# Kernel tuning notes

Measured on AMD Instinct MI355X. Metric: run time of the kernel, lower is better.

## Reference

```python
import jax, jax.numpy as jnp
import numpy as np

HID, FFN, NE, TOPK = 1024, 4096, 8, 2


def setup_inputs() -> dict:
    key = jax.random.key(0)
    ks = jax.random.split(key, 4)
    x = jax.random.normal(ks[0], (2, 2048, HID), dtype=jnp.float32)
    # router: nn.Linear(hidden, num_experts, bias=False), init std=0.02; stored as [H, E]
    Wr = jax.random.normal(ks[1], (HID, NE), dtype=jnp.float32) * 0.02
    # per-expert FFN weights stacked on leading expert axis
    W1 = jax.random.normal(ks[2], (NE, HID, FFN), dtype=jnp.float32) * (1.0 / np.sqrt(HID))
    b1 = jnp.zeros((NE, FFN), dtype=jnp.float32)
    W2 = jax.random.normal(ks[3], (NE, FFN, HID), dtype=jnp.float32) * (1.0 / np.sqrt(FFN))
    b2 = jnp.zeros((NE, HID), dtype=jnp.float32)
    return {"x": x, "Wr": Wr, "W1": W1, "b1": b1, "W2": W2, "b2": b2}


def reference(x, Wr, W1, b1, W2, b2):
    B, S, H = x.shape
    E = Wr.shape[1]
    T = B * S
    xf = x.reshape(T, H)                                  # [T, H]
    logits = xf @ Wr                                      # [T, E]
    probs = jax.nn.softmax(logits, axis=-1)
    topk_p, topk_i = jax.lax.top_k(probs, TOPK)           # [T, K]
    topk_p = topk_p / jnp.sum(topk_p, axis=-1, keepdims=True)
    # dense combine weights: c[t, e] = normalized prob if expert e selected for token t else 0
    c = jnp.zeros((T, E), dtype=xf.dtype).at[jnp.arange(T)[:, None], topk_i].add(topk_p)

    def expert_step(acc, ew):
        w1, bb1, w2, bb2, ce = ew                         # ce: [T]
        h = jax.nn.gelu(xf @ w1 + bb1, approximate=False)  # exact GELU like nn.GELU()
        y = h @ w2 + bb2                                  # [T, H]
        return acc + ce[:, None] * y, None

    out, _ = jax.lax.scan(expert_step, jnp.zeros_like(xf), (W1, b1, W2, b2, c.T))
    return out.reshape(B, S, H)
```

## Files before the change

kernel.cpp:

```cpp
#include <hip/hip_runtime.h>
#include <hip/hip_bf16.h>

#define H 1024
#define F 4096
#define NE 8
#define T 4096
#define KSPLIT2 2

typedef unsigned short u16;
typedef float floatx4 __attribute__((ext_vector_type(4)));
typedef short short8 __attribute__((ext_vector_type(8)));

__device__ __forceinline__ u16 f2bf(float f) {
  union { float f; unsigned int u; } c; c.f = f;
  unsigned int u = c.u;
  return (u16)((u + 0x7fffu + ((u >> 16) & 1u)) >> 16);
}

__device__ __forceinline__ void load16_lds(const u16* g, u16* l) {
  __builtin_amdgcn_global_load_lds(
      (const __attribute__((address_space(1))) unsigned int*)g,
      (__attribute__((address_space(3))) unsigned int*)l, 16, 0, 0);
}

__device__ __forceinline__ float gelu_f(float v) {
  float y = fabsf(v) * 0.70710678118f;
  float t = __builtin_amdgcn_rcpf(fmaf(0.3275911f, y, 1.0f));
  float p = t * fmaf(t, fmaf(t, fmaf(t, fmaf(t, 1.061405429f, -1.453152027f),
                                     1.421413741f), -0.284496736f), 0.254829592f);
  float e = __builtin_amdgcn_exp2f(-y * y * 1.44269504f);
  float erfv = fmaf(-p, e, 1.0f);
  return fmaf(0.5f * fabsf(v), erfv, 0.5f * v);
}

__global__ __launch_bounds__(256) void router_kernel(
    const float* __restrict__ x, const float* __restrict__ Wr,
    int* __restrict__ cnt, int* __restrict__ tok, float* __restrict__ wgt) {
  int t = (blockIdx.x * 256 + threadIdx.x) >> 6;
  int lane = threadIdx.x & 63;
  const float* xr = x + (size_t)t * H;
  double p[NE];
#pragma unroll
  for (int e = 0; e < NE; ++e) p[e] = 0.0;
  for (int k = lane; k < H; k += 64) {
    float xv = xr[k];
    const float4* wr4 = reinterpret_cast<const float4*>(Wr + k * NE);
    float4 a = wr4[0], b = wr4[1];
    p[0] += (double)xv * a.x; p[1] += (double)xv * a.y;
    p[2] += (double)xv * a.z; p[3] += (double)xv * a.w;
    p[4] += (double)xv * b.x; p[5] += (double)xv * b.y;
    p[6] += (double)xv * b.z; p[7] += (double)xv * b.w;
  }
#pragma unroll
  for (int e = 0; e < NE; ++e) {
#pragma unroll
    for (int off = 32; off; off >>= 1) p[e] += __shfl_down(p[e], off, 64);
  }
  if (lane == 0) {
    int i0 = 0;
#pragma unroll
    for (int e = 1; e < NE; ++e) if (p[e] > p[i0]) i0 = e;
    int i1 = (i0 == 0) ? 1 : 0;
#pragma unroll
    for (int e = 0; e < NE; ++e) if (e != i0 && p[e] > p[i1]) i1 = e;
    double d = exp(p[i1] - p[i0]);
    float w0 = (float)(1.0 / (1.0 + d));
    float w1 = (float)(d / (1.0 + d));
    int pos0 = atomicAdd(&cnt[i0], 1);
    tok[i0 * T + pos0] = t; wgt[i0 * T + pos0] = w0;
    int pos1 = atomicAdd(&cnt[i1], 1);
    tok[i1 * T + pos1] = t; wgt[i1 * T + pos1] = w1;
  }
}

__global__ void offsets_kernel(const int* __restrict__ cnt, int* __restrict__ off) {
  if (threadIdx.x == 0) {
    int s = 0;
#pragma unroll
    for (int e = 0; e < NE; ++e) { off[e] = s; s += cnt[e]; }
    off[NE] = s;
  }
}

__global__ __launch_bounds__(256) void convert_x_kernel(
    const float* __restrict__ x, u16* __restrict__ xb) {
  int i = blockIdx.x * 256 + threadIdx.x;
  float4 v = reinterpret_cast<const float4*>(x)[i];
  ushort4 o;
  o.x = f2bf(v.x); o.y = f2bf(v.y); o.z = f2bf(v.z); o.w = f2bf(v.w);
  reinterpret_cast<ushort4*>(xb)[i] = o;
}

__global__ __launch_bounds__(256) void transpose_both_kernel(
    const float* __restrict__ W1, const float* __restrict__ W2,
    u16* __restrict__ W1t, u16* __restrict__ W2t) {
  __shared__ u16 tile[64][72];
  int z = blockIdx.z;
  int e = z & 7;
  const float* s; u16* d; int R, C, c0, r0;
  if (z < NE) {
    s = W1 + (size_t)e * H * F; d = W1t + (size_t)e * H * F;
    R = H; C = F; c0 = blockIdx.x << 6; r0 = blockIdx.y << 6;
  } else {
    s = W2 + (size_t)e * F * H; d = W2t + (size_t)e * F * H;
    R = F; C = H; c0 = blockIdx.y << 6; r0 = blockIdx.x << 6;
  }
  int t = threadIdx.x;
  int rl = t >> 4, cl = (t & 15) << 2;
#pragma unroll
  for (int i = 0; i < 4; ++i) {
    float4 v = *reinterpret_cast<const float4*>(&s[(size_t)(r0 + rl + i * 16) * C + c0 + cl]);
    ushort4 o; o.x = f2bf(v.x); o.y = f2bf(v.y); o.z = f2bf(v.z); o.w = f2bf(v.w);
    *reinterpret_cast<ushort4*>(&tile[rl + i * 16][cl]) = o;
  }
  __syncthreads();
  int cl2 = t >> 4, rl2 = (t & 15) << 2;
#pragma unroll
  for (int i = 0; i < 4; ++i) {
    ushort4 o;
    o.x = tile[rl2 + 0][cl2 + i * 16];
    o.y = tile[rl2 + 1][cl2 + i * 16];
    o.z = tile[rl2 + 2][cl2 + i * 16];
    o.w = tile[rl2 + 3][cl2 + i * 16];
    *reinterpret_cast<ushort4*>(&d[(size_t)(c0 + cl2 + i * 16) * R + r0 + rl2]) = o;
  }
}

__global__ __launch_bounds__(256) void gemm1_kernel(
    const u16* __restrict__ Xb, const u16* __restrict__ W1t,
    const float* __restrict__ b1, const int* __restrict__ cnt,
    const int* __restrict__ off, const int* __restrict__ tok,
    u16* __restrict__ Hc) {
  int e = blockIdx.z;
  int n = cnt[e];
  int m0 = blockIdx.y << 7;
  if (m0 >= n) return;
  int n0 = blockIdx.x << 7;
  int rb = off[e];

  __shared__ alignas(16) u16 As[3][128 * 32];
  __shared__ alignas(16) u16 Bs[3][128 * 32];
  __shared__ int tokS[128];

  int tid = threadIdx.x;
  if (tid < 128) {
    int s = m0 + tid;
    tokS[tid] = (s < n) ? tok[e * T + s] : 0;
  }
  __syncthreads();

  const u16* W1e = W1t + (size_t)e * F * H;
  const u16* aP0 = Xb + (size_t)tokS[tid >> 2] * H + (tid & 3) * 8;
  const u16* aP1 = Xb + (size_t)tokS[64 + (tid >> 2)] * H + (tid & 3) * 8;
  const u16* bP0 = W1e + (size_t)(n0 + (tid >> 2)) * H + (tid & 3) * 8;
  const u16* bP1 = W1e + (size_t)(n0 + 64 + (tid >> 2)) * H + (tid & 3) * 8;

  int wv = tid >> 6, lane = tid & 63;
  int wm = wv >> 1, wn = wv & 1;
  int quad = lane >> 4, l16 = lane & 15;

  floatx4 acc[4][4];
#pragma unroll
  for (int mt = 0; mt < 4; ++mt)
#pragma unroll
    for (int nt = 0; nt < 4; ++nt) acc[mt][nt] = floatx4{0.f, 0.f, 0.f, 0.f};

  int aOff[4], bOff[4];
#pragma unroll
  for (int i = 0; i < 4; ++i) {
    aOff[i] = (wm * 64 + i * 16 + l16) * 32 + quad * 8;
    bOff[i] = (wn * 64 + i * 16 + l16) * 32 + quad * 8;
  }

#define STAGE1(buf, kk)                                   \
  do {                                                    \
    load16_lds(aP0 + (kk), &As[buf][tid * 8]);            \
    load16_lds(aP1 + (kk), &As[buf][(tid + 256) * 8]);    \
    load16_lds(bP0 + (kk), &Bs[buf][tid * 8]);            \
    load16_lds(bP1 + (kk), &Bs[buf][(tid + 256) * 8]);    \
  } while (0)

  const int NIT = H / 32;
  STAGE1(0, 0);
  STAGE1(1, 32);
  for (int it = 0; it < NIT; ++it) {
    if (it == NIT - 1) asm volatile("s_waitcnt vmcnt(0)" ::: "memory");
    else               asm volatile("s_waitcnt vmcnt(4)" ::: "memory");
    __builtin_amdgcn_s_barrier();
    int cur = it % 3;
    if (it + 2 < NIT) STAGE1((it + 2) % 3, (it + 2) * 32);
    short8 av[4], bv[4];
#pragma unroll
    for (int i = 0; i < 4; ++i) {
      av[i] = *reinterpret_cast<const short8*>(&As[cur][aOff[i]]);
      bv[i] = *reinterpret_cast<const short8*>(&Bs[cur][bOff[i]]);
    }
#pragma unroll
    for (int mt = 0; mt < 4; ++mt)
#pragma unroll
      for (int nt = 0; nt < 4; ++nt)
        acc[mt][nt] = __builtin_amdgcn_mfma_f32_16x16x32_bf16(av[mt], bv[nt], acc[mt][nt], 0, 0, 0);
  }
#undef STAGE1

  float b1v[4];
#pragma unroll
  for (int nt = 0; nt < 4; ++nt)
    b1v[nt] = b1[e * F + n0 + wn * 64 + nt * 16 + l16];
#pragma unroll
  for (int mt = 0; mt < 4; ++mt) {
#pragma unroll
    for (int i = 0; i < 4; ++i) {
      int row = wm * 64 + mt * 16 + quad * 4 + i;
      int gr = m0 + row;
      if (gr < n) {
        u16* hrow = Hc + (size_t)(rb + gr) * F + n0 + wn * 64 + l16;
#pragma unroll
        for (int nt = 0; nt < 4; ++nt) {
          float v = acc[mt][nt][i] + b1v[nt];
          hrow[nt * 16] = f2bf(gelu_f(v));
        }
      }
    }
  }
}

__global__ __launch_bounds__(256) void gemm2_kernel(
    const u16* __restrict__ Hc, const u16* __restrict__ W2t,
    const float* __restrict__ b2, const int* __restrict__ cnt,
    const int* __restrict__ off, const int* __restrict__ tok,
    const float* __restrict__ wgt, float* __restrict__ out) {
  int e = blockIdx.z >> 1;
  int kc = blockIdx.z & 1;
  int n = cnt[e];
  int m0 = blockIdx.y << 7;
  if (m0 >= n) return;
  int n0 = blockIdx.x << 7;
  int rb = off[e];

  __shared__ alignas(16) u16 As[3][128 * 32];
  __shared__ alignas(16) u16 Bs[3][128 * 32];

  int tid = threadIdx.x;
  const u16* W2e = W2t + (size_t)e * F * H;
  const u16* aP0 = Hc + (size_t)(rb + m0 + (tid >> 2)) * F + (tid & 3) * 8;
  const u16* aP1 = Hc + (size_t)(rb + m0 + 64 + (tid >> 2)) * F + (tid & 3) * 8;
  const u16* bP0 = W2e + (size_t)(n0 + (tid >> 2)) * F + (tid & 3) * 8;
  const u16* bP1 = W2e + (size_t)(n0 + 64 + (tid >> 2)) * F + (tid & 3) * 8;

  int wv = tid >> 6, lane = tid & 63;
  int wm = wv >> 1, wn = wv & 1;
  int quad = lane >> 4, l16 = lane & 15;

  floatx4 acc[4][4];
#pragma unroll
  for (int mt = 0; mt < 4; ++mt)
#pragma unroll
    for (int nt = 0; nt < 4; ++nt) acc[mt][nt] = floatx4{0.f, 0.f, 0.f, 0.f};

  int aOff[4], bOff[4];
#pragma unroll
  for (int i = 0; i < 4; ++i) {
    aOff[i] = (wm * 64 + i * 16 + l16) * 32 + quad * 8;
    bOff[i] = (wn * 64 + i * 16 + l16) * 32 + quad * 8;
  }

#define STAGE2(buf, kk)                                   \
  do {                                                    \
    load16_lds(aP0 + (kk), &As[buf][tid * 8]);            \
    load16_lds(aP1 + (kk), &As[buf][(tid + 256) * 8]);    \
    load16_lds(bP0 + (kk), &Bs[buf][tid * 8]);            \
    load16_lds(bP1 + (kk), &Bs[buf][(tid + 256) * 8]);    \
  } while (0)

  const int kBeg = kc * (F / KSPLIT2);
  const int NIT = (F / KSPLIT2) / 32;
  STAGE2(0, kBeg);
  STAGE2(1, kBeg + 32);
  for (int it = 0; it < NIT; ++it) {
    if (it == NIT - 1) asm volatile("s_waitcnt vmcnt(0)" ::: "memory");
    else               asm volatile("s_waitcnt vmcnt(4)" ::: "memory");
    __builtin_amdgcn_s_barrier();
    int cur = it % 3;
    if (it + 2 < NIT) STAGE2((it + 2) % 3, kBeg + (it + 2) * 32);
    short8 av[4], bv[4];
#pragma unroll
    for (int i = 0; i < 4; ++i) {
      av[i] = *reinterpret_cast<const short8*>(&As[cur][aOff[i]]);
      bv[i] = *reinterpret_cast<const short8*>(&Bs[cur][bOff[i]]);
    }
#pragma unroll
    for (int mt = 0; mt < 4; ++mt)
#pragma unroll
      for (int nt = 0; nt < 4; ++nt)
        acc[mt][nt] = __builtin_amdgcn_mfma_f32_16x16x32_bf16(av[mt], bv[nt], acc[mt][nt], 0, 0, 0);
  }
#undef STAGE2

  float b2v[4];
#pragma unroll
  for (int nt = 0; nt < 4; ++nt)
    b2v[nt] = (kc == 0) ? b2[e * H + n0 + wn * 64 + nt * 16 + l16] : 0.0f;
#pragma unroll
  for (int mt = 0; mt < 4; ++mt) {
#pragma unroll
    for (int i = 0; i < 4; ++i) {
      int row = wm * 64 + mt * 16 + quad * 4 + i;
      int gr = m0 + row;
      if (gr < n) {
        float wv2 = wgt[e * T + gr];
        int tk = tok[e * T + gr];
        float* orow = out + (size_t)tk * H + n0 + wn * 64 + l16;
#pragma unroll
        for (int nt = 0; nt < 4; ++nt)
          atomicAdd(orow + nt * 16, (acc[mt][nt][i] + b2v[nt]) * wv2);
      }
    }
  }
}

extern "C" void kernel_launch(void* const* d_in, const int* in_sizes, int n_in,
                              void* d_out, int out_size, void* d_ws, size_t ws_size,
                              hipStream_t stream) {
  const float* x  = (const float*)d_in[0];
  const float* Wr = (const float*)d_in[1];
  const float* W1 = (const float*)d_in[2];
  const float* b1 = (const float*)d_in[3];
  const float* W2 = (const float*)d_in[4];
  const float* b2 = (const float*)d_in[5];
  float* out = (float*)d_out;

  char* ws = (char*)d_ws;
  int*   cnt = (int*)(ws + 0);
  int*   off = (int*)(ws + 256);
  int*   tok = (int*)(ws + 4096);
  float* wgt = (float*)(ws + 135168);
  u16*   Xb  = (u16*)(ws + 266240);
  u16*   W1t = (u16*)(ws + 8654848);
  u16*   W2t = (u16*)(ws + 75763712);
  u16*   Hc  = (u16*)(ws + 142872576);

  hipMemsetAsync(cnt, 0, 64, stream);
  hipMemsetAsync(out, 0, (size_t)out_size * sizeof(float), stream);

  router_kernel<<<dim3(T / 4), dim3(256), 0, stream>>>(x, Wr, cnt, tok, wgt);
  offsets_kernel<<<dim3(1), dim3(64), 0, stream>>>(cnt, off);
  convert_x_kernel<<<dim3((T * H / 4) / 256), dim3(256), 0, stream>>>(x, Xb);
  transpose_both_kernel<<<dim3(64, 16, 16), dim3(256), 0, stream>>>(W1, W2, W1t, W2t);
  gemm1_kernel<<<dim3(F / 128, 32, NE), dim3(256), 0, stream>>>(Xb, W1t, b1, cnt, off, tok, Hc);
  gemm2_kernel<<<dim3(H / 128, 32, NE * KSPLIT2), dim3(256), 0, stream>>>(Hc, W2t, b2, cnt, off, tok, wgt, out);
}
```

Baseline: 716.5 us.

## XOR-swizzle LDS tiles and switch GEMMs to double-buffered staging

Both expert GEMM kernels now store each 16-byte k-chunk in LDS at an XOR-swizzled position derived from the row index, and the fragment reads use the matching swizzle. This is meant to remove LDS bank conflicts on the short8 reads. The triple-buffer ring becomes a double buffer that is refilled after a second barrier following the MFMAs. LDS per block drops, which may raise occupancy, but the extra barrier per iteration shortens how far loads can run ahead of compute.

Result: faster. 676.2 us (-5.6%).

```diff
diff --git a/kernel.cpp b/kernel.cpp
--- a/kernel.cpp
+++ b/kernel.cpp
@@ -138,8 +138,8 @@
   int n0 = blockIdx.x << 7;
   int rb = off[e];
 
-  __shared__ alignas(16) u16 As[3][128 * 32];
-  __shared__ alignas(16) u16 Bs[3][128 * 32];
+  __shared__ alignas(16) u16 As[2][128 * 32];
+  __shared__ alignas(16) u16 Bs[2][128 * 32];
   __shared__ int tokS[128];
 
   int tid = threadIdx.x;
@@ -149,11 +149,12 @@
   }
   __syncthreads();
 
+  int kchunk = (((tid & 3) ^ ((tid >> 3) & 3))) * 8;
   const u16* W1e = W1t + (size_t)e * F * H;
-  const u16* aP0 = Xb + (size_t)tokS[tid >> 2] * H + (tid & 3) * 8;
-  const u16* aP1 = Xb + (size_t)tokS[64 + (tid >> 2)] * H + (tid & 3) * 8;
-  const u16* bP0 = W1e + (size_t)(n0 + (tid >> 2)) * H + (tid & 3) * 8;
-  const u16* bP1 = W1e + (size_t)(n0 + 64 + (tid >> 2)) * H + (tid & 3) * 8;
+  const u16* aP0 = Xb + (size_t)tokS[tid >> 2] * H + kchunk;
+  const u16* aP1 = Xb + (size_t)tokS[64 + (tid >> 2)] * H + kchunk;
+  const u16* bP0 = W1e + (size_t)(n0 + (tid >> 2)) * H + kchunk;
+  const u16* bP1 = W1e + (size_t)(n0 + 64 + (tid >> 2)) * H + kchunk;
 
   int wv = tid >> 6, lane = tid & 63;
   int wm = wv >> 1, wn = wv & 1;
@@ -165,11 +166,12 @@
 #pragma unroll
     for (int nt = 0; nt < 4; ++nt) acc[mt][nt] = floatx4{0.f, 0.f, 0.f, 0.f};
 
+  int qa = (quad ^ ((l16 >> 1) & 3)) * 8;
   int aOff[4], bOff[4];
 #pragma unroll
   for (int i = 0; i < 4; ++i) {
-    aOff[i] = (wm * 64 + i * 16 + l16) * 32 + quad * 8;
-    bOff[i] = (wn * 64 + i * 16 + l16) * 32 + quad * 8;
+    aOff[i] = (wm * 64 + i * 16 + l16) * 32 + qa;
+    bOff[i] = (wn * 64 + i * 16 + l16) * 32 + qa;
   }
 
 #define STAGE1(buf, kk)                                   \
@@ -184,11 +186,10 @@
   STAGE1(0, 0);
   STAGE1(1, 32);
   for (int it = 0; it < NIT; ++it) {
-    if (it == NIT - 1) asm volatile("s_waitcnt vmcnt(0)" ::: "memory");
+    if (it >= NIT - 1) asm volatile("s_waitcnt vmcnt(0)" ::: "memory");
     else               asm volatile("s_waitcnt vmcnt(4)" ::: "memory");
     __builtin_amdgcn_s_barrier();
-    int cur = it % 3;
-    if (it + 2 < NIT) STAGE1((it + 2) % 3, (it + 2) * 32);
+    int cur = it & 1;
     short8 av[4], bv[4];
 #pragma unroll
     for (int i = 0; i < 4; ++i) {
@@ -200,6 +201,8 @@
 #pragma unroll
       for (int nt = 0; nt < 4; ++nt)
         acc[mt][nt] = __builtin_amdgcn_mfma_f32_16x16x32_bf16(av[mt], bv[nt], acc[mt][nt], 0, 0, 0);
+    __builtin_amdgcn_s_barrier();
+    if (it + 2 < NIT) STAGE1(cur, (it + 2) * 32);
   }
 #undef STAGE1
 
@@ -238,15 +241,16 @@
   int n0 = blockIdx.x << 7;
   int rb = off[e];
 
-  __shared__ alignas(16) u16 As[3][128 * 32];
-  __shared__ alignas(16) u16 Bs[3][128 * 32];
+  __shared__ alignas(16) u16 As[2][128 * 32];
+  __shared__ alignas(16) u16 Bs[2][128 * 32];
 
   int tid = threadIdx.x;
+  int kchunk = (((tid & 3) ^ ((tid >> 3) & 3))) * 8;
   const u16* W2e = W2t + (size_t)e * F * H;
-  const u16* aP0 = Hc + (size_t)(rb + m0 + (tid >> 2)) * F + (tid & 3) * 8;
-  const u16* aP1 = Hc + (size_t)(rb + m0 + 64 + (tid >> 2)) * F + (tid & 3) * 8;
-  const u16* bP0 = W2e + (size_t)(n0 + (tid >> 2)) * F + (tid & 3) * 8;
-  const u16* bP1 = W2e + (size_t)(n0 + 64 + (tid >> 2)) * F + (tid & 3) * 8;
+  const u16* aP0 = Hc + (size_t)(rb + m0 + (tid >> 2)) * F + kchunk;
+  const u16* aP1 = Hc + (size_t)(rb + m0 + 64 + (tid >> 2)) * F + kchunk;
+  const u16* bP0 = W2e + (size_t)(n0 + (tid >> 2)) * F + kchunk;
+  const u16* bP1 = W2e + (size_t)(n0 + 64 + (tid >> 2)) * F + kchunk;
 
   int wv = tid >> 6, lane = tid & 63;
   int wm = wv >> 1, wn = wv & 1;
@@ -258,11 +262,12 @@
 #pragma unroll
     for (int nt = 0; nt < 4; ++nt) acc[mt][nt] = floatx4{0.f, 0.f, 0.f, 0.f};
 
+  int qa = (quad ^ ((l16 >> 1) & 3)) * 8;
   int aOff[4], bOff[4];
 #pragma unroll
   for (int i = 0; i < 4; ++i) {
-    aOff[i] = (wm * 64 + i * 16 + l16) * 32 + quad * 8;
-    bOff[i] = (wn * 64 + i * 16 + l16) * 32 + quad * 8;
+    aOff[i] = (wm * 64 + i * 16 + l16) * 32 + qa;
+    bOff[i] = (wn * 64 + i * 16 + l16) * 32 + qa;
   }
 
 #define STAGE2(buf, kk)                                   \
@@ -278,11 +283,10 @@
   STAGE2(0, kBeg);
   STAGE2(1, kBeg + 32);
   for (int it = 0; it < NIT; ++it) {
-    if (it == NIT - 1) asm volatile("s_waitcnt vmcnt(0)" ::: "memory");
+    if (it >= NIT - 1) asm volatile("s_waitcnt vmcnt(0)" ::: "memory");
     else               asm volatile("s_waitcnt vmcnt(4)" ::: "memory");
     __builtin_amdgcn_s_barrier();
-    int cur = it % 3;
-    if (it + 2 < NIT) STAGE2((it + 2) % 3, kBeg + (it + 2) * 32);
+    int cur = it & 1;
     short8 av[4], bv[4];
 #pragma unroll
     for (int i = 0; i < 4; ++i) {
@@ -294,6 +298,8 @@
 #pragma unroll
       for (int nt = 0; nt < 4; ++nt)
         acc[mt][nt] = __builtin_amdgcn_mfma_f32_16x16x32_bf16(av[mt], bv[nt], acc[mt][nt], 0, 0, 0);
+    __builtin_amdgcn_s_barrier();
+    if (it + 2 < NIT) STAGE2(cur, kBeg + (it + 2) * 32);
   }
 #undef STAGE2
 
```
